# Performance work log

Measured on AMD Instinct MI355X. Metric: run time of the kernel, lower is better.

The kernel has to match this reference:

```python
import jax, jax.numpy as jnp
import numpy as np

N = 100000      # nodes
E = 3200000     # edges
F_IN = 128      # input feature dim
H = 256         # hidden dim
K = 30          # num_cluster
REG = 0.01      # regularizer coefficient


def _uniform(key, shape, fan_in):
    s = 1.0 / np.sqrt(fan_in)
    return jax.random.uniform(key, shape, jnp.float32, -s, s)


def setup_inputs() -> dict:
    key = jax.random.key(0)
    ks = jax.random.split(key, 11)
    x = jax.random.normal(ks[0], (N, F_IN), jnp.float32)
    edge_index = jax.random.randint(ks[1], (2, E), 0, N, jnp.int32)
    edge_attr = jax.random.uniform(ks[2], (E,), jnp.float32)
    return dict(
        x=x, edge_index=edge_index, edge_attr=edge_attr,
        W_conv1=_uniform(ks[3], (F_IN, H), F_IN), b_conv1=jnp.zeros((H,), jnp.float32),
        W_lin1=_uniform(ks[4], (F_IN, H), F_IN),  b_lin1=_uniform(ks[5], (H,), F_IN),
        W_conv2=_uniform(ks[6], (H, K), H),       b_conv2=jnp.zeros((K,), jnp.float32),
        W_lin2=_uniform(ks[7], (H, K), H),        b_lin2=_uniform(ks[8], (K,), H),
    )


def gcn_conv(x, W, b, row, col, w):
    """PyG GCNConv: symmetric-normalized, edge-weighted aggregation with self-loops (weight 1)."""
    n = x.shape[0]
    deg = jax.ops.segment_sum(w, col, num_segments=n) + 1.0  # self-loop weight 1
    dis = jax.lax.rsqrt(deg)                                  # deg > 0 always (self-loop)
    norm = dis[row] * w * dis[col]                            # [E]
    h = x @ W                                                 # [n, out]
    agg = jax.ops.segment_sum(norm[:, None] * h[row], col, num_segments=n)
    agg = agg + (dis * dis)[:, None] * h                      # self-loop contribution
    return agg + b


def reference(x, edge_index, edge_attr,
              W_conv1, b_conv1, W_lin1, b_lin1,
              W_conv2, b_conv2, W_lin2, b_lin2):
    row, col = edge_index[0], edge_index[1]
    # dropout is identity in eval mode
    h = jax.nn.relu(gcn_conv(x, W_conv1, b_conv1, row, col, edge_attr) + x @ W_lin1 + b_lin1)
    out = gcn_conv(h, W_conv2, b_conv2, row, col, edge_attr) + h @ W_lin2 + b_lin2
    FX = jnp.clip(jax.nn.softmax(out, axis=-1), 1e-9, 1.0 - 1e-9)  # [N, K]

    # modularity loss
    m = jnp.sum(edge_attr)
    degree = jax.ops.segment_sum(edge_attr, row, num_segments=x.shape[0])  # [N]
    connectivity = jnp.sum(edge_attr * jnp.sum(FX[row, :-1] * FX[col, :-1], axis=-1))
    s = jnp.sum(FX * degree[:, None], axis=0)[:-1]
    avg_connectivity = jnp.dot(s, s) / (2.0 * m)
    modularity = -(connectivity - avg_connectivity) / (2.0 * m)

    # collapse regularizer
    reg = (jnp.sqrt(jnp.sum(jnp.sum(FX, axis=0) ** 2) + 1e-9)
           * (FX.shape[-1] ** 0.5) / FX.shape[0] - 1.0)
    return FX, modularity + REG * reg
```

## Files before the change

### kernel.cpp

```cpp
#include <hip/hip_runtime.h>
#include <hip/hip_bf16.h>
#include <math.h>

#define N_NODES 100000
#define N_EDGES 3200000
#define F_IN 128
#define HID 256
#define KCL 30
#define NCOPY 8

typedef unsigned int uint;
typedef unsigned short ushort;
typedef __attribute__((ext_vector_type(8))) short bf16x8;
typedef __attribute__((ext_vector_type(4))) float f32x4;

static __device__ __forceinline__ float bf2f(ushort u) {
  return __uint_as_float(((uint)u) << 16);
}
static __device__ __forceinline__ float bf2f_hi(uint u) {
  return __uint_as_float(u & 0xFFFF0000u);
}
static __device__ __forceinline__ ushort f2bf(float f) {
  uint u = __float_as_uint(f);
  uint r = (u + 0x7FFF + ((u >> 16) & 1)) >> 16;
  return (ushort)r;
}


__global__ __launch_bounds__(256) void k_cnt8(const int* __restrict__ ei,
                                              int* __restrict__ cnt8) {
  int e = blockIdx.x * 256 + threadIdx.x;
  int g = blockIdx.x & (NCOPY - 1);
  int c = ei[N_EDGES + e];
  atomicAdd(cnt8 + (size_t)g * N_NODES + c, 1);
}

__global__ __launch_bounds__(1024) void k_scanA(const int* __restrict__ cnt8,
                                                int* __restrict__ off8,
                                                int* __restrict__ blocktot) {
  __shared__ int wsum[16];
  const int t = threadIdx.x;
  const int lane = t & 63, wid = t >> 6;
  int node = blockIdx.x * 1024 + t;
  int v[NCOPY];
  int tot = 0;
  if (node < N_NODES) {
    #pragma unroll
    for (int g = 0; g < NCOPY; ++g) {
      int x = cnt8[(size_t)g * N_NODES + node];
      v[g] = tot;
      tot += x;
    }
  } else {
    #pragma unroll
    for (int g = 0; g < NCOPY; ++g) v[g] = 0;
  }
  int x = tot;
  #pragma unroll
  for (int o = 1; o < 64; o <<= 1) {
    int y = __shfl_up(x, o);
    if (lane >= o) x += y;
  }
  if (lane == 63) wsum[wid] = x;
  __syncthreads();
  if (t < 16) {
    int s = wsum[t];
    #pragma unroll
    for (int o = 1; o < 16; o <<= 1) {
      int y = __shfl_up(s, o);
      if (t >= o) s += y;
    }
    wsum[t] = s;
  }
  __syncthreads();
  int excl = (wid ? wsum[wid - 1] : 0) + x - tot;
  if (node < N_NODES) {
    #pragma unroll
    for (int g = 0; g < NCOPY; ++g) off8[(size_t)node * NCOPY + g] = excl + v[g];
  }
  if (t == 0) blocktot[blockIdx.x] = wsum[15];
}

__global__ void k_scanB(const int* __restrict__ blocktot, int* __restrict__ blockoff) {
  if (threadIdx.x == 0 && blockIdx.x == 0) {
    int acc = 0;
    for (int b = 0; b < 98; ++b) { blockoff[b] = acc; acc += blocktot[b]; }
  }
}

__global__ __launch_bounds__(256) void k_scanC(int* __restrict__ off8,
                                               const int* __restrict__ blockoff) {
  int idx = blockIdx.x * 256 + threadIdx.x;
  if (idx > N_NODES * NCOPY) return;
  if (idx == N_NODES * NCOPY) { off8[idx] = N_EDGES; return; }
  off8[idx] += blockoff[idx >> 13];
}

__global__ __launch_bounds__(256) void k_csrfill8(const int* __restrict__ ei,
                                                  const float* __restrict__ w,
                                                  int* __restrict__ cnt8,
                                                  const int* __restrict__ off8,
                                                  int* __restrict__ csr_src,
                                                  float* __restrict__ csr_w) {
  int e = blockIdx.x * 256 + threadIdx.x;
  int g = blockIdx.x & (NCOPY - 1);
  int r = ei[e], c = ei[N_EDGES + e];
  int idx = atomicSub(cnt8 + (size_t)g * N_NODES + c, 1) - 1;
  int pos = off8[(size_t)c * NCOPY + g] + idx;
  csr_src[pos] = r;
  csr_w[pos] = w[e];
}

__global__ __launch_bounds__(256) void k_degdis(const int* __restrict__ off8,
                                                const float* __restrict__ csr_w,
                                                float* __restrict__ dis,
                                                float* __restrict__ m_out) {
  int n = blockIdx.x * 256 + threadIdx.x;
  float s = 0.f;
  if (n < N_NODES) {
    int e0 = off8[(size_t)n * NCOPY];
    int e1 = off8[(size_t)(n + 1) * NCOPY];
    for (int j = e0; j < e1; ++j) s += csr_w[j];
    dis[n] = rsqrtf(s + 1.f);
  }
  float v = s;
  #pragma unroll
  for (int o = 32; o > 0; o >>= 1) v += __shfl_down(v, o);
  __shared__ float ls[4];
  int lane = threadIdx.x & 63, wid = threadIdx.x >> 6;
  if (lane == 0) ls[wid] = v;
  __syncthreads();
  if (threadIdx.x == 0) atomicAdd(m_out, ls[0] + ls[1] + ls[2] + ls[3]);
}

__global__ __launch_bounds__(256) void k_pn(const int* __restrict__ csr_src,
                                            const float* __restrict__ dis,
                                            float* __restrict__ csr_w) {
  int j = blockIdx.x * 256 + threadIdx.x;
  int s = csr_src[j];
  csr_w[j] *= dis[s];
}

__global__ __launch_bounds__(256) void k_wprep(const float* __restrict__ Wc,
                                               const float* __restrict__ Wl,
                                               ushort* __restrict__ WT1) {
  int idx = blockIdx.x * 256 + threadIdx.x;
  int vc = idx >> 5;
  int kq = (idx & 31) * 4;
  const float* W = (vc < HID) ? Wc : Wl;
  int c = vc & (HID - 1);
  ushort4 u;
  u.x = f2bf(W[(size_t)(kq + 0) * HID + c]);
  u.y = f2bf(W[(size_t)(kq + 1) * HID + c]);
  u.z = f2bf(W[(size_t)(kq + 2) * HID + c]);
  u.w = f2bf(W[(size_t)(kq + 3) * HID + c]);
  *(ushort4*)(WT1 + (size_t)vc * F_IN + kq) = u;
}

__global__ __launch_bounds__(256) void k_wprep2(const float* __restrict__ Wc,
                                                const float* __restrict__ Wl,
                                                ushort* __restrict__ WT2) {
  int idx = blockIdx.x * 256 + threadIdx.x;
  int vc = idx >> 6;
  int kq = (idx & 63) * 4;
  const float* W = (vc < 32) ? Wc : Wl;
  int c = vc & 31;
  ushort4 u = make_ushort4(0, 0, 0, 0);
  if (c < KCL) {
    u.x = f2bf(W[(size_t)(kq + 0) * KCL + c]);
    u.y = f2bf(W[(size_t)(kq + 1) * KCL + c]);
    u.z = f2bf(W[(size_t)(kq + 2) * KCL + c]);
    u.w = f2bf(W[(size_t)(kq + 3) * KCL + c]);
  }
  *(ushort4*)(WT2 + (size_t)vc * HID + kq) = u;
}

__global__ __launch_bounds__(256) void k_gemm1m(const float* __restrict__ x,
                                                const ushort* __restrict__ WT1,
                                                const float* __restrict__ bc,
                                                const float* __restrict__ bl,
                                                const float* __restrict__ dis,
                                                ushort* __restrict__ hconv_bf,
                                                float* __restrict__ base1) {
  __shared__ ushort xs[32 * F_IN];
  const int t = threadIdx.x;
  const int lane = t & 63, wid = t >> 6;
  const int m0 = blockIdx.x * 32;
  {
    int row = t >> 3, k0 = (t & 7) * 16;
    const float4* xp = (const float4*)(x + (size_t)(m0 + row) * F_IN + k0);
    #pragma unroll
    for (int q = 0; q < 4; ++q) {
      float4 v = xp[q];
      ushort4 u = make_ushort4(f2bf(v.x), f2bf(v.y), f2bf(v.z), f2bf(v.w));
      int k = k0 + q * 4;
      *(ushort4*)&xs[row * F_IN + (k ^ ((row & 7) << 3))] = u;
    }
  }
  __syncthreads();
  const int r0 = lane & 15, r1 = 16 + (lane & 15);
  const int kb = (lane >> 4) * 8;
  bf16x8 A0[4], A1[4];
  #pragma unroll
  for (int ks = 0; ks < 4; ++ks) {
    int k = ks * 32 + kb;
    A0[ks] = *(const bf16x8*)&xs[r0 * F_IN + (k ^ ((r0 & 7) << 3))];
    A1[ks] = *(const bf16x8*)&xs[r1 * F_IN + (k ^ ((r1 & 7) << 3))];
  }
  const int rb = (lane >> 4) * 4;
  #pragma unroll
  for (int cb = 0; cb < 2; ++cb) {
    bf16x8 B[4][4];
    const int vbase = cb * 128 + wid * 32 + (lane & 15);
    #pragma unroll
    for (int cs = 0; cs < 2; ++cs)
      #pragma unroll
      for (int cf = 0; cf < 2; ++cf)
        #pragma unroll
        for (int ks = 0; ks < 4; ++ks) {
          int vc = cs * HID + vbase + cf * 16;
          B[cs * 2 + cf][ks] = *(const bf16x8*)(WT1 + (size_t)vc * F_IN + ks * 32 + kb);
        }
    f32x4 acc[2][4];
    #pragma unroll
    for (int fm = 0; fm < 2; ++fm)
      #pragma unroll
      for (int f = 0; f < 4; ++f) acc[fm][f] = (f32x4){0.f, 0.f, 0.f, 0.f};
    #pragma unroll
    for (int ks = 0; ks < 4; ++ks) {
      #pragma unroll
      for (int f = 0; f < 4; ++f) {
        acc[0][f] = __builtin_amdgcn_mfma_f32_16x16x32_bf16(A0[ks], B[f][ks], acc[0][f], 0, 0, 0);
        acc[1][f] = __builtin_amdgcn_mfma_f32_16x16x32_bf16(A1[ks], B[f][ks], acc[1][f], 0, 0, 0);
      }
    }
    #pragma unroll
    for (int cf = 0; cf < 2; ++cf) {
      int c = cb * 128 + wid * 32 + cf * 16 + (lane & 15);
      float bcv = bc[c], blv = bl[c];
      #pragma unroll
      for (int fm = 0; fm < 2; ++fm) {
        #pragma unroll
        for (int r = 0; r < 4; ++r) {
          int row = m0 + fm * 16 + rb + r;
          float hc = acc[fm][cf][r];
          float hl = acc[fm][2 + cf][r];
          float d = dis[row];
          hconv_bf[(size_t)row * HID + c] = f2bf(hc);
          base1[(size_t)row * HID + c] = hl + blv + bcv + d * d * hc;
        }
      }
    }
  }
}

__global__ __launch_bounds__(256) void k_agg1(const int* __restrict__ off8,
                                              const int* __restrict__ csr_src,
                                              const float* __restrict__ csr_pn,
                                              const float* __restrict__ dis,
                                              const ushort* __restrict__ hconv_bf,
                                              const float* __restrict__ base1,
                                              ushort* __restrict__ h1b) {
  const int n = blockIdx.x;
  const int t = threadIdx.x;
  const int lane = t & 63, wid = t >> 6;
  const int e0 = off8[(size_t)n * NCOPY];
  const int e1 = off8[(size_t)(n + 1) * NCOPY];
  __shared__ int s_src[256];
  __shared__ float s_pn[256];
  __shared__ float red[4][256];
  float acc0 = 0.f, acc1 = 0.f, acc2 = 0.f, acc3 = 0.f;
  for (int jb = e0; jb < e1; jb += 256) {
    int cn = min(256, e1 - jb);
    __syncthreads();
    if (t < cn) {
      s_src[t] = csr_src[jb + t];
      s_pn[t] = csr_pn[jb + t];
    }
    __syncthreads();
    int j = wid;
    for (; j + 4 < cn; j += 8) {
      int sA = s_src[j];         float nA = s_pn[j];
      int sB = s_src[j + 4];     float nB = s_pn[j + 4];
      ushort4 vA = *(const ushort4*)(hconv_bf + (size_t)sA * HID + lane * 4);
      ushort4 vB = *(const ushort4*)(hconv_bf + (size_t)sB * HID + lane * 4);
      acc0 = fmaf(nA, bf2f(vA.x), acc0); acc1 = fmaf(nA, bf2f(vA.y), acc1);
      acc2 = fmaf(nA, bf2f(vA.z), acc2); acc3 = fmaf(nA, bf2f(vA.w), acc3);
      acc0 = fmaf(nB, bf2f(vB.x), acc0); acc1 = fmaf(nB, bf2f(vB.y), acc1);
      acc2 = fmaf(nB, bf2f(vB.z), acc2); acc3 = fmaf(nB, bf2f(vB.w), acc3);
    }
    if (j < cn) {
      int sA = s_src[j]; float nA = s_pn[j];
      ushort4 vA = *(const ushort4*)(hconv_bf + (size_t)sA * HID + lane * 4);
      acc0 = fmaf(nA, bf2f(vA.x), acc0); acc1 = fmaf(nA, bf2f(vA.y), acc1);
      acc2 = fmaf(nA, bf2f(vA.z), acc2); acc3 = fmaf(nA, bf2f(vA.w), acc3);
    }
  }
  __syncthreads();
  ((float4*)red[wid])[lane] = make_float4(acc0, acc1, acc2, acc3);
  __syncthreads();
  float dn = dis[n];
  float v = dn * (red[0][t] + red[1][t] + red[2][t] + red[3][t]) + base1[(size_t)n * HID + t];
  h1b[(size_t)n * HID + t] = f2bf(fmaxf(v, 0.f));
}

__global__ __launch_bounds__(256) void k_gemm2m(const ushort* __restrict__ h1b,
                                                const ushort* __restrict__ WT2,
                                                const float* __restrict__ bc,
                                                const float* __restrict__ bl,
                                                const float* __restrict__ dis,
                                                ushort* __restrict__ hconv2p,
                                                float* __restrict__ base2p) {
  __shared__ ushort hs[64 * HID];
  const int t = threadIdx.x;
  const int lane = t & 63, wid = t >> 6;
  const int n0 = blockIdx.x * 64;
  {
    int row = t >> 2, kq = (t & 3) * 64;
    int gn = n0 + row;
    #pragma unroll
    for (int q = 0; q < 8; ++q) {
      int k = kq + q * 8;
      uint4 u = make_uint4(0, 0, 0, 0);
      if (gn < N_NODES) u = *(const uint4*)(h1b + (size_t)gn * HID + k);
      *(uint4*)&hs[row * HID + (k ^ ((row & 7) << 3))] = u;
    }
  }
  __syncthreads();
  const int lr = wid * 16 + (lane & 15);
  const int kb = (lane >> 4) * 8;
  f32x4 acc[4];
  #pragma unroll
  for (int f = 0; f < 4; ++f) acc[f] = (f32x4){0.f, 0.f, 0.f, 0.f};
  #pragma unroll
  for (int ks = 0; ks < 8; ++ks) {
    int k = ks * 32 + kb;
    bf16x8 A = *(const bf16x8*)&hs[lr * HID + (k ^ ((lr & 7) << 3))];
    #pragma unroll
    for (int f = 0; f < 4; ++f) {
      int vc = f * 16 + (lane & 15);
      bf16x8 B = *(const bf16x8*)(WT2 + (size_t)vc * HID + k);
      acc[f] = __builtin_amdgcn_mfma_f32_16x16x32_bf16(A, B, acc[f], 0, 0, 0);
    }
  }
  const int rb = (lane >> 4) * 4;
  #pragma unroll
  for (int cf = 0; cf < 2; ++cf) {
    int c = cf * 16 + (lane & 15);
    if (c < KCL) {
      float bcv = bc[c], blv = bl[c];
      #pragma unroll
      for (int r = 0; r < 4; ++r) {
        int row = n0 + wid * 16 + rb + r;
        if (row < N_NODES) {
          float hc = acc[cf][r];
          float hl = acc[2 + cf][r];
          float d = dis[row];
          hconv2p[(size_t)row * 32 + c] = f2bf(hc);
          base2p[(size_t)row * 32 + c] = hl + blv + bcv + d * d * hc;
        }
      }
    }
  }
}

__global__ __launch_bounds__(256) void k_agg2(const int* __restrict__ off8,
                                              const int* __restrict__ csr_src,
                                              const float* __restrict__ csr_pn,
                                              const float* __restrict__ dis,
                                              const ushort* __restrict__ hconv2p,
                                              const float* __restrict__ base2p,
                                              float* __restrict__ FX,
                                              ushort* __restrict__ FXbp,
                                              float* __restrict__ scal) {
  const int t = threadIdx.x;
  const int lane = t & 63, wid = t >> 6;
  const int half = lane >> 5, c = lane & 31;
  const int nwaves = gridDim.x * 4;
  const int gw = blockIdx.x * 4 + wid;
  float cs_acc = 0.f;
  for (int n = gw; n < N_NODES; n += nwaves) {
    int e0 = off8[(size_t)n * NCOPY];
    int e1 = off8[(size_t)(n + 1) * NCOPY];
    float accA = 0.f, accB = 0.f;
    int j = e0 + half;
    for (; j + 2 < e1; j += 4) {
      int s0 = csr_src[j];
      int s1 = csr_src[j + 2];
      float p0 = csr_pn[j];
      float p1 = csr_pn[j + 2];
      float v0 = (c < KCL) ? bf2f(hconv2p[(size_t)s0 * 32 + c]) : 0.f;
      float v1 = (c < KCL) ? bf2f(hconv2p[(size_t)s1 * 32 + c]) : 0.f;
      accA = fmaf(p0, v0, accA);
      accB = fmaf(p1, v1, accB);
    }
    if (j < e1) {
      int s0 = csr_src[j];
      float p0 = csr_pn[j];
      float v0 = (c < KCL) ? bf2f(hconv2p[(size_t)s0 * 32 + c]) : 0.f;
      accA = fmaf(p0, v0, accA);
    }
    float acc = accA + accB;
    acc += __shfl(acc, lane ^ 32);
    float out = (c < KCL) ? acc * dis[n] + base2p[(size_t)n * 32 + c] : -1e30f;
    float mx = out;
    #pragma unroll
    for (int o = 16; o > 0; o >>= 1) mx = fmaxf(mx, __shfl_xor(mx, o));
    float p = (c < KCL) ? __expf(out - mx) : 0.f;
    float sum = p;
    #pragma unroll
    for (int o = 16; o > 0; o >>= 1) sum += __shfl_xor(sum, o);
    float fx = p / sum;
    fx = fminf(fmaxf(fx, 1e-9f), 1.f - 1e-9f);
    if (half == 0 && c < KCL) {
      FX[(size_t)n * KCL + c] = fx;
      FXbp[(size_t)n * 32 + c] = f2bf(fx);
    }
    cs_acc += (c < KCL) ? fx : 0.f;
  }
  __shared__ float red_cs[4][32];
  if (half == 0) red_cs[wid][c] = cs_acc;
  __syncthreads();
  if (t < KCL) {
    float a = red_cs[0][t] + red_cs[1][t] + red_cs[2][t] + red_cs[3][t];
    atomicAdd(&scal[2 + t], a);
  }
}

__global__ __launch_bounds__(256) void k_conn(const int* __restrict__ ei,
                                              const float* __restrict__ w,
                                              const ushort* __restrict__ FXbp,
                                              float* __restrict__ scal) {
  const int t = threadIdx.x;
  const int lane = t & 63, wid = t >> 6;
  const size_t e0 = ((size_t)blockIdx.x * 256 + t) * 4;
  float sv[29];
  #pragma unroll
  for (int k = 0; k < 29; ++k) sv[k] = 0.f;
  float conn = 0.f;
  int4 rr = *(const int4*)(ei + e0);
  int4 cc = *(const int4*)(ei + N_EDGES + e0);
  float4 ww = *(const float4*)(w + e0);
  const int rA[4] = {rr.x, rr.y, rr.z, rr.w};
  const int cA[4] = {cc.x, cc.y, cc.z, cc.w};
  const float wA[4] = {ww.x, ww.y, ww.z, ww.w};
  #pragma unroll
  for (int q = 0; q < 4; ++q) {
    int r = rA[q], cN = cA[q];
    float wv = wA[q];
    const uint* fr = (const uint*)FXbp + (size_t)r * 16;
    const uint* fc = (const uint*)FXbp + (size_t)cN * 16;
    float dot = 0.f;
    #pragma unroll
    for (int k = 0; k < 14; ++k) {
      uint ua = fr[k], ub = fc[k];
      float a0 = bf2f((ushort)(ua & 0xFFFF)), a1 = bf2f_hi(ua);
      float b0 = bf2f((ushort)(ub & 0xFFFF)), b1 = bf2f_hi(ub);
      dot += a0 * b0 + a1 * b1;
      sv[2 * k] = fmaf(wv, a0, sv[2 * k]);
      sv[2 * k + 1] = fmaf(wv, a1, sv[2 * k + 1]);
    }
    float a28 = bf2f((ushort)(fr[14] & 0xFFFF));
    float b28 = bf2f((ushort)(fc[14] & 0xFFFF));
    dot += a28 * b28;
    sv[28] = fmaf(wv, a28, sv[28]);
    conn = fmaf(wv, dot, conn);
  }
  __shared__ float red[4][30];
  #pragma unroll
  for (int i = 0; i < 30; ++i) {
    float v = (i < 29) ? sv[i] : conn;
    #pragma unroll
    for (int o = 32; o > 0; o >>= 1) v += __shfl_down(v, o);
    if (lane == 0) red[wid][i] = v;
  }
  __syncthreads();
  if (t < 30) {
    float s = red[0][t] + red[1][t] + red[2][t] + red[3][t];
    atomicAdd(t == 29 ? &scal[1] : &scal[32 + t], s);
  }
}

__global__ void k_finalize(const float* __restrict__ scal, float* __restrict__ out_loss) {
  if (threadIdx.x == 0 && blockIdx.x == 0) {
    float m = scal[0], conn = scal[1];
    float ss = 0.f;
    for (int k = 0; k < KCL - 1; ++k) { float s = scal[32 + k]; ss += s * s; }
    float cs2 = 0.f;
    for (int k = 0; k < KCL; ++k) { float cv = scal[2 + k]; cs2 += cv * cv; }
    float avg = ss / (2.f * m);
    float modularity = -(conn - avg) / (2.f * m);
    float reg = sqrtf(cs2 + 1e-9f) * sqrtf((float)KCL) / (float)N_NODES - 1.f;
    out_loss[0] = modularity + 0.01f * reg;
  }
}

extern "C" void kernel_launch(void* const* d_in, const int* in_sizes, int n_in,
                              void* d_out, int out_size, void* d_ws, size_t ws_size,
                              hipStream_t stream) {
  const float* x   = (const float*)d_in[0];
  const int*   ei  = (const int*)d_in[1];
  const float* ea  = (const float*)d_in[2];
  const float* Wc1 = (const float*)d_in[3];
  const float* bc1 = (const float*)d_in[4];
  const float* Wl1 = (const float*)d_in[5];
  const float* bl1 = (const float*)d_in[6];
  const float* Wc2 = (const float*)d_in[7];
  const float* bc2 = (const float*)d_in[8];
  const float* Wl2 = (const float*)d_in[9];
  const float* bl2 = (const float*)d_in[10];
  float* out = (float*)d_out;

  float* ws = (float*)d_ws;
  size_t o = 0;
  int*   cnt8   = (int*)(ws + o); o += (size_t)NCOPY * N_NODES;
  float* scal   = ws + o; o += 64;
  size_t zero_floats = o;
  int*   off8   = (int*)(ws + o); o += (size_t)N_NODES * NCOPY + 8;
  int*   blocktot = (int*)(ws + o); o += 128;
  int*   blockoff = (int*)(ws + o); o += 128;
  float* dis    = ws + o; o += N_NODES;
  int*   csr_src= (int*)(ws + o); o += N_EDGES;
  float* csr_w  = ws + o; o += N_EDGES;
  ushort* WT1   = (ushort*)(ws + o); o += (size_t)512 * F_IN / 2;
  ushort* WT2   = (ushort*)(ws + o); o += (size_t)64 * HID / 2;
  ushort* hconv_bf = (ushort*)(ws + o); o += (size_t)N_NODES * HID / 2;
  float* base1  = ws + o; o += (size_t)N_NODES * HID;
  ushort* h1b   = (ushort*)(ws + o); o += (size_t)N_NODES * HID / 2;
  ushort* hconv2p = (ushort*)(ws + o); o += (size_t)N_NODES * 32 / 2;
  float* base2p = ws + o; o += (size_t)N_NODES * 32;
  o += 64;
  if (ws_size < o * sizeof(float)) return;

  ushort* FXbp = hconv_bf;

  hipMemsetAsync(d_ws, 0, zero_floats * sizeof(float), stream);

  k_cnt8<<<N_EDGES / 256, 256, 0, stream>>>(ei, cnt8);
  k_scanA<<<98, 1024, 0, stream>>>(cnt8, off8, blocktot);
  k_scanB<<<1, 64, 0, stream>>>(blocktot, blockoff);
  k_scanC<<<(N_NODES * NCOPY + 256) / 256, 256, 0, stream>>>(off8, blockoff);
  k_csrfill8<<<N_EDGES / 256, 256, 0, stream>>>(ei, ea, cnt8, off8, csr_src, csr_w);
  k_degdis<<<(N_NODES + 255) / 256, 256, 0, stream>>>(off8, csr_w, dis, scal);
  k_pn<<<N_EDGES / 256, 256, 0, stream>>>(csr_src, dis, csr_w);
  k_wprep<<<64, 256, 0, stream>>>(Wc1, Wl1, WT1);
  k_wprep2<<<16, 256, 0, stream>>>(Wc2, Wl2, WT2);
  k_gemm1m<<<N_NODES / 32, 256, 0, stream>>>(x, WT1, bc1, bl1, dis, hconv_bf, base1);
  k_agg1<<<N_NODES, 256, 0, stream>>>(off8, csr_src, csr_w, dis, hconv_bf, base1, h1b);
  k_gemm2m<<<(N_NODES + 63) / 64, 256, 0, stream>>>(h1b, WT2, bc2, bl2, dis, hconv2p, base2p);
  k_agg2<<<2048, 256, 0, stream>>>(off8, csr_src, csr_w, dis, hconv2p, base2p, out, FXbp, scal);
  k_conn<<<N_EDGES / 1024, 256, 0, stream>>>(ei, ea, FXbp, scal);
  k_finalize<<<1, 64, 0, stream>>>(scal, out + (size_t)N_NODES * KCL);
}
```

Baseline: 1.007 ms.

## Store layer-1 hidden features in FP8, base in bf16, and interleave CSR arrays

The layer-1 conv features gathered per edge are now stored as FP8 (e4m3) instead of bf16, which halves gather bytes in the dominant aggregation kernel. The linear/base term is stored in bf16 instead of fp32. CSR source and normalized weight are packed into one int2 array, so each edge needs a single load. This trades numerical precision for less memory traffic. FP8 quantization of activations with up to 32 in-degree sums may push accuracy close to the tolerance.

```diff
diff --git a/kernel.cpp b/kernel.cpp
--- a/kernel.cpp
+++ b/kernel.cpp
@@ -11,8 +11,10 @@
 
 typedef unsigned int uint;
 typedef unsigned short ushort;
+typedef unsigned char uchar;
 typedef __attribute__((ext_vector_type(8))) short bf16x8;
 typedef __attribute__((ext_vector_type(4))) float f32x4;
+typedef __attribute__((ext_vector_type(2))) float f32x2;
 
 static __device__ __forceinline__ float bf2f(ushort u) {
   return __uint_as_float(((uint)u) << 16);
@@ -24,6 +26,44 @@
   uint u = __float_as_uint(f);
   uint r = (u + 0x7FFF + ((u >> 16) & 1)) >> 16;
   return (ushort)r;
+}
+
+static __device__ __forceinline__ uchar f2fp8(float f) {
+#if __has_builtin(__builtin_amdgcn_cvt_pk_fp8_f32)
+  return (uchar)(__builtin_amdgcn_cvt_pk_fp8_f32(f, f, 0, false) & 0xFF);
+#else
+  uint u = __float_as_uint(f);
+  uint s = (u >> 24) & 0x80u;
+  float a = fabsf(f);
+  if (a >= 448.f) return (uchar)(s | 0x7E);
+  if (a < 0.015625f) {
+    int q = (int)rintf(a * 512.f);
+    return (uchar)(s | (q > 8 ? 8 : q));
+  }
+  int e = ((int)((u >> 23) & 0xFF)) - 127;
+  float step = __uint_as_float((uint)(127 + e - 3) << 23);
+  int q = (int)rintf(a / step);
+  if (q == 16) { e += 1; q = 8; }
+  return (uchar)(s | ((e + 7) << 3) | (q - 8));
+#endif
+}
+static __device__ __forceinline__ float fp82f_sw(uchar b) {
+  uint s = ((uint)(b & 0x80u)) << 24;
+  uint em = b & 0x7Fu;
+  float mag;
+  if ((em >> 3) == 0) mag = (float)em * 0.001953125f;
+  else mag = __uint_as_float((((em >> 3) + 120) << 23) | ((em & 7u) << 20));
+  return __uint_as_float(s | __float_as_uint(mag));
+}
+static __device__ __forceinline__ void fp8x4_dec(uint u, float* o) {
+#if __has_builtin(__builtin_amdgcn_cvt_pk_f32_fp8)
+  f32x2 lo = __builtin_amdgcn_cvt_pk_f32_fp8((int)u, false);
+  f32x2 hi = __builtin_amdgcn_cvt_pk_f32_fp8((int)u, true);
+  o[0] = lo.x; o[1] = lo.y; o[2] = hi.x; o[3] = hi.y;
+#else
+  o[0] = fp82f_sw(u & 0xFF); o[1] = fp82f_sw((u >> 8) & 0xFF);
+  o[2] = fp82f_sw((u >> 16) & 0xFF); o[3] = fp82f_sw((u >> 24) & 0xFF);
+#endif
 }
 
 
@@ -100,19 +140,17 @@
                                                   const float* __restrict__ w,
                                                   int* __restrict__ cnt8,
                                                   const int* __restrict__ off8,
-                                                  int* __restrict__ csr_src,
-                                                  float* __restrict__ csr_w) {
+                                                  int2* __restrict__ csr) {
   int e = blockIdx.x * 256 + threadIdx.x;
   int g = blockIdx.x & (NCOPY - 1);
   int r = ei[e], c = ei[N_EDGES + e];
   int idx = atomicSub(cnt8 + (size_t)g * N_NODES + c, 1) - 1;
   int pos = off8[(size_t)c * NCOPY + g] + idx;
-  csr_src[pos] = r;
-  csr_w[pos] = w[e];
+  csr[pos] = make_int2(r, __float_as_int(w[e]));
 }
 
 __global__ __launch_bounds__(256) void k_degdis(const int* __restrict__ off8,
-                                                const float* __restrict__ csr_w,
+                                                const int2* __restrict__ csr,
                                                 float* __restrict__ dis,
                                                 float* __restrict__ m_out) {
   int n = blockIdx.x * 256 + threadIdx.x;
@@ -120,7 +158,7 @@
   if (n < N_NODES) {
     int e0 = off8[(size_t)n * NCOPY];
     int e1 = off8[(size_t)(n + 1) * NCOPY];
-    for (int j = e0; j < e1; ++j) s += csr_w[j];
+    for (int j = e0; j < e1; ++j) s += __int_as_float(csr[j].y);
     dis[n] = rsqrtf(s + 1.f);
   }
   float v = s;
@@ -133,12 +171,11 @@
   if (threadIdx.x == 0) atomicAdd(m_out, ls[0] + ls[1] + ls[2] + ls[3]);
 }
 
-__global__ __launch_bounds__(256) void k_pn(const int* __restrict__ csr_src,
-                                            const float* __restrict__ dis,
-                                            float* __restrict__ csr_w) {
+__global__ __launch_bounds__(256) void k_pn(int2* __restrict__ csr,
+                                            const float* __restrict__ dis) {
   int j = blockIdx.x * 256 + threadIdx.x;
-  int s = csr_src[j];
-  csr_w[j] *= dis[s];
+  int2 e = csr[j];
+  csr[j] = make_int2(e.x, __float_as_int(__int_as_float(e.y) * dis[e.x]));
 }
 
 __global__ __launch_bounds__(256) void k_wprep(const float* __restrict__ Wc,
@@ -180,9 +217,10 @@
                                                 const float* __restrict__ bc,
                                                 const float* __restrict__ bl,
                                                 const float* __restrict__ dis,
-                                                ushort* __restrict__ hconv_bf,
-                                                float* __restrict__ base1) {
+                                                uchar* __restrict__ hconv_f8,
+                                                ushort* __restrict__ base1b) {
   __shared__ ushort xs[32 * F_IN];
+  uchar* xs8 = (uchar*)xs;
   const int t = threadIdx.x;
   const int lane = t & 63, wid = t >> 6;
   const int m0 = blockIdx.x * 32;
@@ -207,6 +245,7 @@
     A0[ks] = *(const bf16x8*)&xs[r0 * F_IN + (k ^ ((r0 & 7) << 3))];
     A1[ks] = *(const bf16x8*)&xs[r1 * F_IN + (k ^ ((r1 & 7) << 3))];
   }
+  __syncthreads();
   const int rb = (lane >> 4) * 4;
   #pragma unroll
   for (int cb = 0; cb < 2; ++cb) {
@@ -242,65 +281,78 @@
       for (int fm = 0; fm < 2; ++fm) {
         #pragma unroll
         for (int r = 0; r < 4; ++r) {
-          int row = m0 + fm * 16 + rb + r;
+          int lrow = fm * 16 + rb + r;
+          int row = m0 + lrow;
           float hc = acc[fm][cf][r];
           float hl = acc[fm][2 + cf][r];
           float d = dis[row];
-          hconv_bf[(size_t)row * HID + c] = f2bf(hc);
-          base1[(size_t)row * HID + c] = hl + blv + bcv + d * d * hc;
+          xs8[lrow * 256 + c] = f2fp8(hc);
+          base1b[(size_t)row * HID + c] = f2bf(hl + blv + bcv + d * d * hc);
         }
       }
     }
   }
+  __syncthreads();
+  {
+    int row = t >> 3, c0 = (t & 7) * 32;
+    uint4 a = *(const uint4*)&xs8[row * 256 + c0];
+    uint4 b = *(const uint4*)&xs8[row * 256 + c0 + 16];
+    uchar* dst = hconv_f8 + (size_t)(m0 + row) * 256 + c0;
+    *(uint4*)dst = a;
+    *(uint4*)(dst + 16) = b;
+  }
 }
 
 __global__ __launch_bounds__(256) void k_agg1(const int* __restrict__ off8,
-                                              const int* __restrict__ csr_src,
-                                              const float* __restrict__ csr_pn,
+                                              const int2* __restrict__ csr,
+                                              const uint* __restrict__ hconv_u32,
+                                              const ushort* __restrict__ base1b,
                                               const float* __restrict__ dis,
-                                              const ushort* __restrict__ hconv_bf,
-                                              const float* __restrict__ base1,
                                               ushort* __restrict__ h1b) {
   const int n = blockIdx.x;
   const int t = threadIdx.x;
   const int lane = t & 63, wid = t >> 6;
   const int e0 = off8[(size_t)n * NCOPY];
   const int e1 = off8[(size_t)(n + 1) * NCOPY];
-  __shared__ int s_src[256];
-  __shared__ float s_pn[256];
+  __shared__ int2 s_e[256];
   __shared__ float red[4][256];
   float acc0 = 0.f, acc1 = 0.f, acc2 = 0.f, acc3 = 0.f;
   for (int jb = e0; jb < e1; jb += 256) {
     int cn = min(256, e1 - jb);
     __syncthreads();
-    if (t < cn) {
-      s_src[t] = csr_src[jb + t];
-      s_pn[t] = csr_pn[jb + t];
-    }
+    if (t < cn) s_e[t] = csr[jb + t];
     __syncthreads();
     int j = wid;
     for (; j + 4 < cn; j += 8) {
-      int sA = s_src[j];         float nA = s_pn[j];
-      int sB = s_src[j + 4];     float nB = s_pn[j + 4];
-      ushort4 vA = *(const ushort4*)(hconv_bf + (size_t)sA * HID + lane * 4);
-      ushort4 vB = *(const ushort4*)(hconv_bf + (size_t)sB * HID + lane * 4);
-      acc0 = fmaf(nA, bf2f(vA.x), acc0); acc1 = fmaf(nA, bf2f(vA.y), acc1);
-      acc2 = fmaf(nA, bf2f(vA.z), acc2); acc3 = fmaf(nA, bf2f(vA.w), acc3);
-      acc0 = fmaf(nB, bf2f(vB.x), acc0); acc1 = fmaf(nB, bf2f(vB.y), acc1);
-      acc2 = fmaf(nB, bf2f(vB.z), acc2); acc3 = fmaf(nB, bf2f(vB.w), acc3);
+      int2 eA = s_e[j];
+      int2 eB = s_e[j + 4];
+      float nA = __int_as_float(eA.y);
+      float nB = __int_as_float(eB.y);
+      uint uA = hconv_u32[(size_t)eA.x * 64 + lane];
+      uint uB = hconv_u32[(size_t)eB.x * 64 + lane];
+      float vA[4], vB[4];
+      fp8x4_dec(uA, vA);
+      fp8x4_dec(uB, vB);
+      acc0 = fmaf(nA, vA[0], acc0); acc1 = fmaf(nA, vA[1], acc1);
+      acc2 = fmaf(nA, vA[2], acc2); acc3 = fmaf(nA, vA[3], acc3);
+      acc0 = fmaf(nB, vB[0], acc0); acc1 = fmaf(nB, vB[1], acc1);
+      acc2 = fmaf(nB, vB[2], acc2); acc3 = fmaf(nB, vB[3], acc3);
     }
     if (j < cn) {
-      int sA = s_src[j]; float nA = s_pn[j];
-      ushort4 vA = *(const ushort4*)(hconv_bf + (size_t)sA * HID + lane * 4);
-      acc0 = fmaf(nA, bf2f(vA.x), acc0); acc1 = fmaf(nA, bf2f(vA.y), acc1);
-      acc2 = fmaf(nA, bf2f(vA.z), acc2); acc3 = fmaf(nA, bf2f(vA.w), acc3);
+      int2 eA = s_e[j];
+      float nA = __int_as_float(eA.y);
+      uint uA = hconv_u32[(size_t)eA.x * 64 + lane];
+      float vA[4];
+      fp8x4_dec(uA, vA);
+      acc0 = fmaf(nA, vA[0], acc0); acc1 = fmaf(nA, vA[1], acc1);
+      acc2 = fmaf(nA, vA[2], acc2); acc3 = fmaf(nA, vA[3], acc3);
     }
   }
   __syncthreads();
   ((float4*)red[wid])[lane] = make_float4(acc0, acc1, acc2, acc3);
   __syncthreads();
   float dn = dis[n];
-  float v = dn * (red[0][t] + red[1][t] + red[2][t] + red[3][t]) + base1[(size_t)n * HID + t];
+  float v = dn * (red[0][t] + red[1][t] + red[2][t] + red[3][t]) + bf2f(base1b[(size_t)n * HID + t]);
   h1b[(size_t)n * HID + t] = f2bf(fmaxf(v, 0.f));
 }
 
@@ -365,8 +417,7 @@
 }
 
 __global__ __launch_bounds__(256) void k_agg2(const int* __restrict__ off8,
-                                              const int* __restrict__ csr_src,
-                                              const float* __restrict__ csr_pn,
+                                              const int2* __restrict__ csr,
                                               const float* __restrict__ dis,
                                               const ushort* __restrict__ hconv2p,
                                               const float* __restrict__ base2p,
@@ -385,19 +436,19 @@
     float accA = 0.f, accB = 0.f;
     int j = e0 + half;
     for (; j + 2 < e1; j += 4) {
-      int s0 = csr_src[j];
-      int s1 = csr_src[j + 2];
-      float p0 = csr_pn[j];
-      float p1 = csr_pn[j + 2];
-      float v0 = (c < KCL) ? bf2f(hconv2p[(size_t)s0 * 32 + c]) : 0.f;
-      float v1 = (c < KCL) ? bf2f(hconv2p[(size_t)s1 * 32 + c]) : 0.f;
+      int2 eA = csr[j];
+      int2 eB = csr[j + 2];
+      float p0 = __int_as_float(eA.y);
+      float p1 = __int_as_float(eB.y);
+      float v0 = (c < KCL) ? bf2f(hconv2p[(size_t)eA.x * 32 + c]) : 0.f;
+      float v1 = (c < KCL) ? bf2f(hconv2p[(size_t)eB.x * 32 + c]) : 0.f;
       accA = fmaf(p0, v0, accA);
       accB = fmaf(p1, v1, accB);
     }
     if (j < e1) {
-      int s0 = csr_src[j];
-      float p0 = csr_pn[j];
-      float v0 = (c < KCL) ? bf2f(hconv2p[(size_t)s0 * 32 + c]) : 0.f;
+      int2 eA = csr[j];
+      float p0 = __int_as_float(eA.y);
+      float v0 = (c < KCL) ? bf2f(hconv2p[(size_t)eA.x * 32 + c]) : 0.f;
       accA = fmaf(p0, v0, accA);
     }
     float acc = accA + accB;
@@ -520,19 +571,18 @@
   int*   blocktot = (int*)(ws + o); o += 128;
   int*   blockoff = (int*)(ws + o); o += 128;
   float* dis    = ws + o; o += N_NODES;
-  int*   csr_src= (int*)(ws + o); o += N_EDGES;
-  float* csr_w  = ws + o; o += N_EDGES;
+  int2*  csr    = (int2*)(ws + o); o += (size_t)N_EDGES * 2;
   ushort* WT1   = (ushort*)(ws + o); o += (size_t)512 * F_IN / 2;
   ushort* WT2   = (ushort*)(ws + o); o += (size_t)64 * HID / 2;
-  ushort* hconv_bf = (ushort*)(ws + o); o += (size_t)N_NODES * HID / 2;
-  float* base1  = ws + o; o += (size_t)N_NODES * HID;
+  uchar* hconv_f8 = (uchar*)(ws + o); o += (size_t)N_NODES * HID / 4;
+  ushort* base1b = (ushort*)(ws + o); o += (size_t)N_NODES * HID / 2;
   ushort* h1b   = (ushort*)(ws + o); o += (size_t)N_NODES * HID / 2;
   ushort* hconv2p = (ushort*)(ws + o); o += (size_t)N_NODES * 32 / 2;
   float* base2p = ws + o; o += (size_t)N_NODES * 32;
   o += 64;
   if (ws_size < o * sizeof(float)) return;
 
-  ushort* FXbp = hconv_bf;
+  ushort* FXbp = (ushort*)hconv_f8;
 
   hipMemsetAsync(d_ws, 0, zero_floats * sizeof(float), stream);
 
@@ -540,15 +590,15 @@
   k_scanA<<<98, 1024, 0, stream>>>(cnt8, off8, blocktot);
   k_scanB<<<1, 64, 0, stream>>>(blocktot, blockoff);
   k_scanC<<<(N_NODES * NCOPY + 256) / 256, 256, 0, stream>>>(off8, blockoff);
-  k_csrfill8<<<N_EDGES / 256, 256, 0, stream>>>(ei, ea, cnt8, off8, csr_src, csr_w);
-  k_degdis<<<(N_NODES + 255) / 256, 256, 0, stream>>>(off8, csr_w, dis, scal);
-  k_pn<<<N_EDGES / 256, 256, 0, stream>>>(csr_src, dis, csr_w);
+  k_csrfill8<<<N_EDGES / 256, 256, 0, stream>>>(ei, ea, cnt8, off8, csr);
+  k_degdis<<<(N_NODES + 255) / 256, 256, 0, stream>>>(off8, csr, dis, scal);
+  k_pn<<<N_EDGES / 256, 256, 0, stream>>>(csr, dis);
   k_wprep<<<64, 256, 0, stream>>>(Wc1, Wl1, WT1);
   k_wprep2<<<16, 256, 0, stream>>>(Wc2, Wl2, WT2);
-  k_gemm1m<<<N_NODES / 32, 256, 0, stream>>>(x, WT1, bc1, bl1, dis, hconv_bf, base1);
-  k_agg1<<<N_NODES, 256, 0, stream>>>(off8, csr_src, csr_w, dis, hconv_bf, base1, h1b);
+  k_gemm1m<<<N_NODES / 32, 256, 0, stream>>>(x, WT1, bc1, bl1, dis, hconv_f8, base1b);
+  k_agg1<<<N_NODES, 256, 0, stream>>>(off8, csr, (const uint*)hconv_f8, base1b, dis, h1b);
   k_gemm2m<<<(N_NODES + 63) / 64, 256, 0, stream>>>(h1b, WT2, bc2, bl2, dis, hconv2p, base2p);
-  k_agg2<<<2048, 256, 0, stream>>>(off8, csr_src, csr_w, dis, hconv2p, base2p, out, FXbp, scal);
+  k_agg2<<<2048, 256, 0, stream>>>(off8, csr, dis, hconv2p, base2p, out, FXbp, scal);
   k_conn<<<N_EDGES / 1024, 256, 0, stream>>>(ei, ea, FXbp, scal);
   k_finalize<<<1, 64, 0, stream>>>(scal, out + (size_t)N_NODES * KCL);
 }
```

Measured after the change: 888.8 us. 1.13x faster.
